# Kernel optimization log

Hardware: AMD Instinct MI355X
Metric: run time of the kernel (lower is better)

## Reference

```python
import jax, jax.numpy as jnp
import numpy as np
from jax import lax

THRESH = 0.6      # pnet score threshold (threshold[0])
IOU_THR = 0.5     # per-scale nms threshold in detect_face
K_PICKS = 128     # fixed max number of NMS picks (jit-static)
STRIDE = 2.0
CELL = 12.0
NEG = -1e30


def _conv(x, w, b):
    y = lax.conv_general_dilated(x, w, (1, 1), 'VALID',
                                 dimension_numbers=('NCHW', 'OIHW', 'NCHW'))
    return y + b[None, :, None, None]


def _prelu(x, a):
    return jnp.where(x > 0, x, a[None, :, None, None] * x)


def _maxpool2(x):
    return lax.reduce_window(x, -jnp.inf, lax.max, (1, 1, 2, 2), (1, 1, 2, 2), 'VALID')


def _nms(boxes, scores):
    # Greedy union-IoU NMS (nms_numpy math), vectorized with a fixed pick budget.
    # boxes [N,4] (shared grid), scores [N] with invalid entries already = NEG.
    x1, y1, x2, y2 = boxes[:, 0], boxes[:, 1], boxes[:, 2], boxes[:, 3]
    area = (x2 - x1 + 1.0) * (y2 - y1 + 1.0)

    def body(live, _):
        j = jnp.argmax(live)
        s = live[j]
        ok = s > NEG * 0.5
        xx1 = jnp.maximum(x1[j], x1); yy1 = jnp.maximum(y1[j], y1)
        xx2 = jnp.minimum(x2[j], x2); yy2 = jnp.minimum(y2[j], y2)
        inter = jnp.maximum(0.0, xx2 - xx1 + 1.0) * jnp.maximum(0.0, yy2 - yy1 + 1.0)
        iou = inter / (area[j] + area - inter)
        live = jnp.where(iou > IOU_THR, NEG, live).at[j].set(NEG)
        return live, (j, ok)

    _, (idx, ok) = lax.scan(body, scores, None, length=K_PICKS)
    return idx, ok


def setup_inputs():
    key = jax.random.key(0)
    ks = jax.random.split(key, 16)
    B, H, W = 16, 384, 512
    f = lambda k, shp, s=0.1: jax.random.normal(k, shp, jnp.float32) * s
    return {
        'im_data': jax.random.uniform(ks[0], (B, 3, H, W), jnp.float32) * 255.0,
        'c1_w': f(ks[1], (10, 3, 3, 3)), 'c1_b': f(ks[2], (10,)),
        'p1': jnp.full((10,), 0.25, jnp.float32),
        'c2_w': f(ks[3], (16, 10, 3, 3)), 'c2_b': f(ks[4], (16,)),
        'p2': jnp.full((16,), 0.25, jnp.float32),
        'c3_w': f(ks[5], (32, 16, 3, 3)), 'c3_b': f(ks[6], (32,)),
        'p3': jnp.full((32,), 0.25, jnp.float32),
        'c41_w': f(ks[7], (2, 32, 1, 1)), 'c41_b': f(ks[8], (2,)),
        'c42_w': f(ks[9], (4, 32, 1, 1)), 'c42_b': f(ks[10], (4,)),
    }


def reference(im_data, c1_w, c1_b, p1, c2_w, c2_b, p2, c3_w, c3_b, p3,
              c41_w, c41_b, c42_w, c42_b):
    # --- PNet conv trunk (detect_face normalization + MTCNN PNet) ---
    x = (im_data - 127.5) * 0.0078125
    h = _prelu(_conv(x, c1_w, c1_b), p1)
    h = _maxpool2(h)                                   # 2x2 s2 (dims even -> ceil==floor)
    h = _prelu(_conv(h, c2_w, c2_b), p2)
    h = _prelu(_conv(h, c3_w, c3_b), p3)
    probs = jax.nn.softmax(_conv(h, c41_w, c41_b), axis=1)[:, 1]   # [B,Hp,Wp]
    reg = _conv(h, c42_w, c42_b)                                   # [B,4,Hp,Wp]

    # --- generateBoundingBox (dense, masked instead of nonzero; scale=1) ---
    B, Hp, Wp = probs.shape
    yy, xx = jnp.meshgrid(jnp.arange(Hp, dtype=jnp.float32),
                          jnp.arange(Wp, dtype=jnp.float32), indexing='ij')
    boxes4 = jnp.stack([jnp.floor(STRIDE * xx + 1.0).ravel(),
                        jnp.floor(STRIDE * yy + 1.0).ravel(),
                        jnp.floor(STRIDE * xx + CELL).ravel(),
                        jnp.floor(STRIDE * yy + CELL).ravel()], axis=1)  # [N,4]
    scores = probs.reshape(B, -1)                                   # [B,N]
    regf = reg.reshape(B, 4, -1).transpose(0, 2, 1)                 # [B,N,4]
    masked = jnp.where(scores >= THRESH, scores, NEG)

    # --- per-image greedy NMS (batched_nms: images independent) ---
    idx, ok = jax.vmap(_nms, in_axes=(None, 0))(boxes4, masked)     # [B,K]
    pb = boxes4[idx]                                                # [B,K,4]
    ps = jnp.take_along_axis(scores, idx, axis=1)                   # [B,K]
    pr = jnp.take_along_axis(regf, idx[..., None], axis=1)          # [B,K,4]

    w = pb[..., 2] - pb[..., 0]
    hh = pb[..., 3] - pb[..., 1]
    q1 = pb[..., 0] + pr[..., 0] * w
    q2 = pb[..., 1] + pr[..., 1] * hh
    q3 = pb[..., 2] + pr[..., 2] * w
    q4 = pb[..., 3] + pr[..., 3] * hh
    rw = q3 - q1
    rh = q4 - q2
    l = jnp.maximum(rw, rh)
    nx1 = q1 + rw * 0.5 - l * 0.5
    ny1 = q2 + rh * 0.5 - l * 0.5
    out = jnp.stack([nx1, ny1, nx1 + l, ny1 + l, ps], axis=-1)      # [B,K,5]
    return out * ok[..., None].astype(out.dtype)
```

## Files before the change

### kernel.cpp

```cpp
#include <hip/hip_runtime.h>
#include <math.h>

#define BATCH 16
#define IH 384
#define IW 512
#define C1 10
#define P1H 191
#define P1W 255
#define C2 16
#define H2 189
#define W2 253
#define C3 32
#define H3 187
#define W3 251
#define N3 (H3*W3)
#define KP 128
#define CAP 7680
#define NEGV (-1e30f)

typedef _Float16 f16x8 __attribute__((ext_vector_type(8)));
typedef _Float16 f16x4 __attribute__((ext_vector_type(4)));
typedef float    f32x16 __attribute__((ext_vector_type(16)));

#define PXT 98
#define NSUB 3

__global__ __launch_bounds__(256, 2) void k_conv1pool(
        const float* __restrict__ im, const float* __restrict__ w,
        const float* __restrict__ bia, const float* __restrict__ slope,
        float* __restrict__ outp) {
    int x = blockIdx.x * 16 + threadIdx.x;
    int y = blockIdx.y * 16 + threadIdx.y;
    int bb = blockIdx.z;
    if (x >= P1W || y >= P1H) return;

    float in[3][4][4];
    #pragma unroll
    for (int ci = 0; ci < 3; ++ci) {
        const float* p = im + (((size_t)bb * 3 + ci) * IH + 2 * y) * IW + 2 * x;
        #pragma unroll
        for (int r = 0; r < 4; ++r) {
            const float2* q = (const float2*)(p + (size_t)r * IW);
            float2 a0 = q[0], a1 = q[1];
            in[ci][r][0] = a0.x; in[ci][r][1] = a0.y;
            in[ci][r][2] = a1.x; in[ci][r][3] = a1.y;
        }
    }
    #pragma unroll
    for (int ci = 0; ci < 3; ++ci)
        #pragma unroll
        for (int r = 0; r < 4; ++r)
            #pragma unroll
            for (int c = 0; c < 4; ++c)
                in[ci][r][c] = (in[ci][r][c] - 127.5f) * 0.0078125f;

    #pragma unroll
    for (int oc = 0; oc < C1; ++oc) {
        const float* wo = w + oc * 27;
        float bv = bia[oc], sv = slope[oc];
        float best = -INFINITY;
        #pragma unroll
        for (int py = 0; py < 2; ++py)
            #pragma unroll
            for (int px = 0; px < 2; ++px) {
                float acc = bv;
                #pragma unroll
                for (int ci = 0; ci < 3; ++ci)
                    #pragma unroll
                    for (int ky = 0; ky < 3; ++ky)
                        #pragma unroll
                        for (int kx = 0; kx < 3; ++kx)
                            acc += in[ci][py + ky][px + kx] * wo[(ci * 3 + ky) * 3 + kx];
                float v = acc > 0.f ? acc : sv * acc;
                best = fmaxf(best, v);
            }
        outp[(((size_t)bb * C1 + oc) * P1H + y) * P1W + x] = best;
    }
}

__global__ __launch_bounds__(256, 2) void k_conv2(
        const float* __restrict__ inp, const float* __restrict__ w,
        const float* __restrict__ bia, const float* __restrict__ slope,
        float* __restrict__ outp) {
    int x0 = (blockIdx.x * 64 + threadIdx.x) * 2;
    int y  = blockIdx.y * 4 + threadIdx.y;
    int bb = blockIdx.z;
    if (x0 >= W2 || y >= H2) return;

    float a0[C2], a1[C2];
    #pragma unroll
    for (int oc = 0; oc < C2; ++oc) { a0[oc] = bia[oc]; a1[oc] = bia[oc]; }

    bool tail = (x0 + 3 > P1W - 1);

    for (int ci = 0; ci < C1; ++ci) {
        const float* p = inp + (((size_t)bb * C1 + ci) * P1H + y) * P1W + x0;
        float v[3][4];
        #pragma unroll
        for (int r = 0; r < 3; ++r) {
            const float* pr = p + (size_t)r * P1W;
            v[r][0] = pr[0]; v[r][1] = pr[1]; v[r][2] = pr[2];
            v[r][3] = tail ? 0.f : pr[3];
        }
        const float* wc = w + ci * 9;
        #pragma unroll
        for (int oc = 0; oc < C2; ++oc) {
            const float* wo = wc + oc * (C1 * 9);
            float s0 = a0[oc], s1 = a1[oc];
            #pragma unroll
            for (int ky = 0; ky < 3; ++ky)
                #pragma unroll
                for (int kx = 0; kx < 3; ++kx) {
                    float wv = wo[ky * 3 + kx];
                    s0 += v[ky][kx]     * wv;
                    s1 += v[ky][kx + 1] * wv;
                }
            a0[oc] = s0; a1[oc] = s1;
        }
    }
    #pragma unroll
    for (int oc = 0; oc < C2; ++oc) {
        float sl = slope[oc];
        float u0 = a0[oc]; a0[oc] = u0 > 0.f ? u0 : sl * u0;
        float u1 = a1[oc]; a1[oc] = u1 > 0.f ? u1 : sl * u1;
    }
    float* o = outp + (((size_t)bb * H2 + y) * W2 + x0) * C2;
    float4* o4 = (float4*)o;
    o4[0] = make_float4(a0[0],  a0[1],  a0[2],  a0[3]);
    o4[1] = make_float4(a0[4],  a0[5],  a0[6],  a0[7]);
    o4[2] = make_float4(a0[8],  a0[9],  a0[10], a0[11]);
    o4[3] = make_float4(a0[12], a0[13], a0[14], a0[15]);
    if (x0 + 1 < W2) {
        float4* p4 = (float4*)(o + C2);
        p4[0] = make_float4(a1[0],  a1[1],  a1[2],  a1[3]);
        p4[1] = make_float4(a1[4],  a1[5],  a1[6],  a1[7]);
        p4[2] = make_float4(a1[8],  a1[9],  a1[10], a1[11]);
        p4[3] = make_float4(a1[12], a1[13], a1[14], a1[15]);
    }
}

__global__ __launch_bounds__(256) void k_prep(const float* __restrict__ w3,
                                              _Float16* __restrict__ wbuf) {
    for (int e = threadIdx.x; e < 4608; e += 256) {
        int oc = e / 144;
        int rem = e - oc * 144;
        int ic = rem / 9;
        int tap = rem - ic * 9;
        float v = w3[e];
        _Float16 h = (_Float16)v;
        _Float16 l = (_Float16)(v - (float)h);
        int d = (tap * 32 + oc) * 16 + ic;
        wbuf[d] = h;
        wbuf[4608 + d] = l;
    }
}

__global__ __launch_bounds__(256, 2) void k_conv3mfma(
        const float* __restrict__ act,
        const _Float16* __restrict__ wbuf,
        const float* __restrict__ b3, const float* __restrict__ s3,
        const float* __restrict__ w41, const float* __restrict__ b41,
        const float* __restrict__ w42, const float* __restrict__ b42,
        float* __restrict__ scores, float4* __restrict__ regf) {
    __shared__ __align__(16) _Float16 Whl[2 * 4608];
    __shared__ __align__(16) _Float16 Ah[6 * PXT * 16];
    __shared__ __align__(16) _Float16 Al[6 * PXT * 16];
    __shared__ __align__(16) float    htab[32 * 8];

    int tid = threadIdx.x;
    int bx = blockIdx.x * (NSUB * 32);
    int by = blockIdx.y * 4;
    int bb = blockIdx.z;

    {
        const float4* src = (const float4*)wbuf;
        float4* dst = (float4*)Whl;
        for (int i = tid; i < 1152; i += 256) dst[i] = src[i];
    }
    {
        int oc = tid >> 3, f = tid & 7;
        float v;
        if      (f == 0) v = b3[oc];
        else if (f == 1) v = s3[oc];
        else if (f == 2) v = w41[oc];
        else if (f == 3) v = w41[32 + oc];
        else             v = w42[(f - 4) * 32 + oc];
        htab[tid] = v;
    }
    {
        const float* actb = act + (size_t)bb * H2 * W2 * C2;
        for (int e = tid; e < 6 * PXT * 4; e += 256) {
            int ic4 = e & 3;
            int t = e >> 2;
            int px = t % PXT;
            int row = t / PXT;
            int yg = by + row, xg = bx + px;
            float4 v = make_float4(0.f, 0.f, 0.f, 0.f);
            if (yg < H2 && xg < W2)
                v = *(const float4*)(actb + ((size_t)yg * W2 + xg) * C2 + ic4 * 4);
            float xs0 = v.x, xs1 = v.y, xs2 = v.z, xs3 = v.w;
            f16x4 hv, lv;
            _Float16 h;
            h = (_Float16)xs0; hv[0] = h; lv[0] = (_Float16)(xs0 - (float)h);
            h = (_Float16)xs1; hv[1] = h; lv[1] = (_Float16)(xs1 - (float)h);
            h = (_Float16)xs2; hv[2] = h; lv[2] = (_Float16)(xs2 - (float)h);
            h = (_Float16)xs3; hv[3] = h; lv[3] = (_Float16)(xs3 - (float)h);
            int d = (row * PXT + px) * 16 + ic4 * 4;
            *(f16x4*)(Ah + d) = hv;
            *(f16x4*)(Al + d) = lv;
        }
    }
    __syncthreads();

    int wv = tid >> 6, lane = tid & 63;
    int col = lane & 31, half = lane >> 5, kg8 = half * 8;
    int y = by + wv;
    if (y >= H3) return;

    f32x16 acc[NSUB];
    #pragma unroll
    for (int s = 0; s < NSUB; ++s)
        #pragma unroll
        for (int i = 0; i < 16; ++i) acc[s][i] = 0.f;

    #pragma unroll
    for (int ky = 0; ky < 3; ++ky) {
        const _Float16* arh = Ah + (wv + ky) * (PXT * 16);
        const _Float16* arl = Al + (wv + ky) * (PXT * 16);
        #pragma unroll
        for (int kx = 0; kx < 3; ++kx) {
            int tap = ky * 3 + kx;
            f16x8 wh = *(const f16x8*)(Whl + (tap * 32 + col) * 16 + kg8);
            f16x8 wl = *(const f16x8*)(Whl + 4608 + (tap * 32 + col) * 16 + kg8);
            #pragma unroll
            for (int s = 0; s < NSUB; ++s) {
                int p = s * 32 + col + kx;
                f16x8 bh = *(const f16x8*)(arh + p * 16 + kg8);
                f16x8 bl = *(const f16x8*)(arl + p * 16 + kg8);
                acc[s] = __builtin_amdgcn_mfma_f32_32x32x16_f16(wh, bh, acc[s], 0, 0, 0);
                acc[s] = __builtin_amdgcn_mfma_f32_32x32x16_f16(wl, bh, acc[s], 0, 0, 0);
                acc[s] = __builtin_amdgcn_mfma_f32_32x32x16_f16(wh, bl, acc[s], 0, 0, 0);
            }
        }
    }

    float L0[NSUB], L1[NSUB], R0[NSUB], R1[NSUB], R2[NSUB], R3[NSUB];
    #pragma unroll
    for (int s = 0; s < NSUB; ++s) { L0[s]=0.f; L1[s]=0.f; R0[s]=0.f; R1[s]=0.f; R2[s]=0.f; R3[s]=0.f; }

    #pragma unroll
    for (int r = 0; r < 16; ++r) {
        int oc = (r & 3) + 8 * (r >> 2) + 4 * half;
        float4 t0 = *(const float4*)&htab[oc * 8];
        float4 t1 = *(const float4*)&htab[oc * 8 + 4];
        #pragma unroll
        for (int s = 0; s < NSUB; ++s) {
            float v = acc[s][r] + t0.x;
            v = v > 0.f ? v : v * t0.y;
            L0[s] += v * t0.z; L1[s] += v * t0.w;
            R0[s] += v * t1.x; R1[s] += v * t1.y;
            R2[s] += v * t1.z; R3[s] += v * t1.w;
        }
    }

    float hb0 = b41[0], hb1 = b41[1];
    float rb0 = b42[0], rb1 = b42[1], rb2 = b42[2], rb3 = b42[3];

    #pragma unroll
    for (int s = 0; s < NSUB; ++s) {
        float l0 = L0[s] + __shfl_xor(L0[s], 32) + hb0;
        float l1 = L1[s] + __shfl_xor(L1[s], 32) + hb1;
        float r0 = R0[s] + __shfl_xor(R0[s], 32) + rb0;
        float r1 = R1[s] + __shfl_xor(R1[s], 32) + rb1;
        float r2 = R2[s] + __shfl_xor(R2[s], 32) + rb2;
        float r3 = R3[s] + __shfl_xor(R3[s], 32) + rb3;
        float m = fmaxf(l0, l1);
        float e0 = expf(l0 - m), e1 = expf(l1 - m);
        float p = e1 / (e0 + e1);
        int px = bx + s * 32 + col;
        if (half == 0 && px < W3) {
            size_t n = (size_t)bb * N3 + (size_t)y * W3 + px;
            scores[n] = (p >= 0.6f) ? p : NEGV;
            regf[n] = make_float4(r0, r1, r2, r3);
        }
    }
}

__global__ __launch_bounds__(1024) void k_nms(
        const float* __restrict__ scores, const float4* __restrict__ regf,
        float* __restrict__ outp) {
    __shared__ float s_score[CAP];
    __shared__ int   s_idx[CAP];
    __shared__ float r_s[16];
    __shared__ int   r_i[16];
    __shared__ float s_picks[KP];
    __shared__ int   s_picki[KP];
    __shared__ int   s_misc[4];

    int tid = threadIdx.x;
    int bb = blockIdx.x;
    const float* sc = scores + (size_t)bb * N3;

    if (tid < 4) s_misc[tid] = 0;
    __syncthreads();

    int cnt = 0;
    for (int i = tid; i < N3; i += 1024) if (sc[i] > 0.f) cnt++;
    atomicAdd(&s_misc[0], cnt);
    __syncthreads();
    int M = s_misc[0];

    int cutbin = 0;
    if (M > CAP) {
        for (int i = tid; i < 2048; i += 1024) s_idx[i] = 0;
        __syncthreads();
        for (int i = tid; i < N3; i += 1024) {
            float s = sc[i];
            if (s > 0.f) {
                int b = (int)((s - 0.6f) * 5120.f);
                b = b < 0 ? 0 : (b > 2047 ? 2047 : b);
                atomicAdd(&s_idx[b], 1);
            }
        }
        __syncthreads();
        if (tid == 0) {
            int accum = 0, b = 2047;
            for (; b >= 0; --b) {
                int c = s_idx[b];
                if (accum + c > CAP) break;
                accum += c;
            }
            s_misc[2] = b + 1;
        }
        __syncthreads();
        cutbin = s_misc[2];
        __syncthreads();
    }

    for (int i = tid; i < N3; i += 1024) {
        float s = sc[i];
        if (s > 0.f) {
            bool keep = true;
            if (M > CAP) {
                int b = (int)((s - 0.6f) * 5120.f);
                b = b < 0 ? 0 : (b > 2047 ? 2047 : b);
                keep = (b >= cutbin);
            }
            if (keep) {
                int pos = atomicAdd(&s_misc[1], 1);
                if (pos < CAP) { s_score[pos] = s; s_idx[pos] = i; }
            }
        }
    }
    __syncthreads();
    int M2 = s_misc[1]; if (M2 > CAP) M2 = CAP;

    int np = 0;
    for (int pick = 0; pick < KP; ++pick) {
        float bs = -INFINITY; int bi = 0x7fffffff;
        for (int i = tid; i < M2; i += 1024) {
            float s = s_score[i]; int id = s_idx[i];
            if (s > bs || (s == bs && id < bi)) { bs = s; bi = id; }
        }
        #pragma unroll
        for (int off = 32; off; off >>= 1) {
            float os = __shfl_down(bs, off);
            int   oi = __shfl_down(bi, off);
            if (os > bs || (os == bs && oi < bi)) { bs = os; bi = oi; }
        }
        int lane = tid & 63, wv = tid >> 6;
        if (lane == 0) { r_s[wv] = bs; r_i[wv] = bi; }
        __syncthreads();
        if (tid == 0) {
            float ps = r_s[0]; int pi = r_i[0];
            for (int k = 1; k < 16; ++k) {
                float os = r_s[k]; int oi = r_i[k];
                if (os > ps || (os == ps && oi < pi)) { ps = os; pi = oi; }
            }
            s_picks[pick] = ps; s_picki[pick] = pi;
            r_s[0] = ps; r_i[0] = pi;
        }
        __syncthreads();
        float ps = r_s[0]; int pi = r_i[0];
        if (ps < 0.f) break;
        np = pick + 1;

        int pcx = pi % W3, pcy = pi / W3;
        float px1 = (float)(2 * pcx + 1), py1 = (float)(2 * pcy + 1);
        float px2 = (float)(2 * pcx + 12), py2 = (float)(2 * pcy + 12);
        for (int i = tid; i < M2; i += 1024) {
            float s = s_score[i];
            if (s > NEGV * 0.5f) {
                int id = s_idx[i];
                int cx = id % W3, cy = id / W3;
                float x1 = (float)(2 * cx + 1), y1 = (float)(2 * cy + 1);
                float x2 = (float)(2 * cx + 12), y2 = (float)(2 * cy + 12);
                float xx1 = fmaxf(px1, x1), yy1 = fmaxf(py1, y1);
                float xx2 = fminf(px2, x2), yy2 = fminf(py2, y2);
                float inter = fmaxf(0.f, xx2 - xx1 + 1.f) * fmaxf(0.f, yy2 - yy1 + 1.f);
                float iou = inter / (288.f - inter);
                if (iou > 0.5f) s_score[i] = NEGV;
            }
        }
        __syncthreads();
    }

    if (tid < KP) {
        float* o = outp + ((size_t)bb * KP + tid) * 5;
        if (tid < np) {
            int pi = s_picki[tid]; float ps = s_picks[tid];
            int cx = pi % W3, cy = pi / W3;
            float x1 = (float)(2 * cx + 1), y1 = (float)(2 * cy + 1);
            float x2 = (float)(2 * cx + 12), y2 = (float)(2 * cy + 12);
            float4 r = regf[(size_t)bb * N3 + pi];
            float wd = x2 - x1, hh = y2 - y1;
            float q1 = x1 + r.x * wd, q2 = y1 + r.y * hh;
            float q3 = x2 + r.z * wd, q4 = y2 + r.w * hh;
            float rw = q3 - q1, rh = q4 - q2;
            float L = fmaxf(rw, rh);
            float nx1 = q1 + rw * 0.5f - L * 0.5f;
            float ny1 = q2 + rh * 0.5f - L * 0.5f;
            o[0] = nx1; o[1] = ny1; o[2] = nx1 + L; o[3] = ny1 + L; o[4] = ps;
        } else {
            o[0] = 0.f; o[1] = 0.f; o[2] = 0.f; o[3] = 0.f; o[4] = 0.f;
        }
    }
}

extern "C" void kernel_launch(void* const* d_in, const int* in_sizes, int n_in,
                              void* d_out, int out_size, void* d_ws, size_t ws_size,
                              hipStream_t stream) {
    const float* im   = (const float*)d_in[0];
    const float* c1w  = (const float*)d_in[1];
    const float* c1b  = (const float*)d_in[2];
    const float* p1   = (const float*)d_in[3];
    const float* c2w  = (const float*)d_in[4];
    const float* c2b  = (const float*)d_in[5];
    const float* p2   = (const float*)d_in[6];
    const float* c3w  = (const float*)d_in[7];
    const float* c3b  = (const float*)d_in[8];
    const float* p3   = (const float*)d_in[9];
    const float* c41w = (const float*)d_in[10];
    const float* c41b = (const float*)d_in[11];
    const float* c42w = (const float*)d_in[12];
    const float* c42b = (const float*)d_in[13];

    float* ws = (float*)d_ws;
    const size_t POOL1_FLOATS = (size_t)BATCH * C1 * P1H * P1W;
    float*  pool1  = ws;
    float*  conv2b = ws + POOL1_FLOATS;
    float*  scoresb = ws;
    float4* regfb   = (float4*)(ws + (size_t)BATCH * N3);
    _Float16* wbuf = (_Float16*)d_out;

    k_prep<<<dim3(1), dim3(256), 0, stream>>>(c3w, wbuf);
    k_conv1pool<<<dim3(16, 12, BATCH), dim3(16, 16), 0, stream>>>(im, c1w, c1b, p1, pool1);
    k_conv2   <<<dim3(2, 48, BATCH), dim3(64, 4), 0, stream>>>(pool1, c2w, c2b, p2, conv2b);
    k_conv3mfma<<<dim3(3, 47, BATCH), dim3(256), 0, stream>>>(conv2b, wbuf, c3b, p3,
                                                              c41w, c41b, c42w, c42b,
                                                              scoresb, regfb);
    k_nms<<<dim3(BATCH), dim3(1024), 0, stream>>>(scoresb, regfb, (float*)d_out);
}
```

Before: 244.8 us.

## Fuse weight prep into conv1, stage conv2 stores via LDS, stream conv3 weights from global

The separate weight-prep launch is folded into the first block of conv1, removing one kernel launch. conv2 now stages its outputs through a swizzled shared buffer so global stores are coalesced float4 writes. conv3 stops copying the split-f16 weights into LDS and reads them straight from global memory in a new k-split layout. Activation LDS is reorganised to match, which frees shared memory and raises occupancy to 4 blocks, at the cost of global weight loads inside the MFMA loop and a non-unrolled ky loop.

```diff
diff --git a/kernel.cpp b/kernel.cpp
--- a/kernel.cpp
+++ b/kernel.cpp
@@ -28,7 +28,24 @@
 __global__ __launch_bounds__(256, 2) void k_conv1pool(
         const float* __restrict__ im, const float* __restrict__ w,
         const float* __restrict__ bia, const float* __restrict__ slope,
-        float* __restrict__ outp) {
+        float* __restrict__ outp,
+        const float* __restrict__ w3, _Float16* __restrict__ wbuf) {
+    if (blockIdx.x == 0 && blockIdx.y == 0 && blockIdx.z == 0) {
+        int tid = threadIdx.y * 16 + threadIdx.x;
+        for (int e = tid; e < 4608; e += 256) {
+            int oc = e / 144;
+            int rem = e - oc * 144;
+            int ic = rem / 9;
+            int tap = rem - ic * 9;
+            float v = w3[e];
+            _Float16 h = (_Float16)v;
+            _Float16 l = (_Float16)(v - (float)h);
+            int d = ((tap * 2 + (ic >> 3)) * 32 + oc) * 8 + (ic & 7);
+            wbuf[d] = h;
+            wbuf[4608 + d] = l;
+        }
+    }
+
     int x = blockIdx.x * 16 + threadIdx.x;
     int y = blockIdx.y * 16 + threadIdx.y;
     int bb = blockIdx.z;
@@ -82,89 +99,86 @@
         const float* __restrict__ inp, const float* __restrict__ w,
         const float* __restrict__ bia, const float* __restrict__ slope,
         float* __restrict__ outp) {
-    int x0 = (blockIdx.x * 64 + threadIdx.x) * 2;
-    int y  = blockIdx.y * 4 + threadIdx.y;
+    __shared__ float4 sbuf[2048];
+    int tx = threadIdx.x, ty = threadIdx.y;
+    int tid = ty * 64 + tx;
+    int x0 = blockIdx.x * 128 + tx * 2;
+    int y  = blockIdx.y * 4 + ty;
     int bb = blockIdx.z;
-    if (x0 >= W2 || y >= H2) return;
+    bool alive = (x0 < W2) && (y < H2);
 
     float a0[C2], a1[C2];
     #pragma unroll
     for (int oc = 0; oc < C2; ++oc) { a0[oc] = bia[oc]; a1[oc] = bia[oc]; }
 
-    bool tail = (x0 + 3 > P1W - 1);
-
-    for (int ci = 0; ci < C1; ++ci) {
-        const float* p = inp + (((size_t)bb * C1 + ci) * P1H + y) * P1W + x0;
-        float v[3][4];
-        #pragma unroll
-        for (int r = 0; r < 3; ++r) {
-            const float* pr = p + (size_t)r * P1W;
-            v[r][0] = pr[0]; v[r][1] = pr[1]; v[r][2] = pr[2];
-            v[r][3] = tail ? 0.f : pr[3];
-        }
-        const float* wc = w + ci * 9;
+    if (alive) {
+        bool tail = (x0 + 3 > P1W - 1);
+        for (int ci = 0; ci < C1; ++ci) {
+            const float* p = inp + (((size_t)bb * C1 + ci) * P1H + y) * P1W + x0;
+            float v[3][4];
+            #pragma unroll
+            for (int r = 0; r < 3; ++r) {
+                const float* pr = p + (size_t)r * P1W;
+                v[r][0] = pr[0]; v[r][1] = pr[1]; v[r][2] = pr[2];
+                v[r][3] = tail ? 0.f : pr[3];
+            }
+            const float* wc = w + ci * 9;
+            #pragma unroll
+            for (int oc = 0; oc < C2; ++oc) {
+                const float* wo = wc + oc * (C1 * 9);
+                float s0 = a0[oc], s1 = a1[oc];
+                #pragma unroll
+                for (int ky = 0; ky < 3; ++ky)
+                    #pragma unroll
+                    for (int kx = 0; kx < 3; ++kx) {
+                        float wv = wo[ky * 3 + kx];
+                        s0 += v[ky][kx]     * wv;
+                        s1 += v[ky][kx + 1] * wv;
+                    }
+                a0[oc] = s0; a1[oc] = s1;
+            }
+        }
         #pragma unroll
         for (int oc = 0; oc < C2; ++oc) {
-            const float* wo = wc + oc * (C1 * 9);
-            float s0 = a0[oc], s1 = a1[oc];
-            #pragma unroll
-            for (int ky = 0; ky < 3; ++ky)
-                #pragma unroll
-                for (int kx = 0; kx < 3; ++kx) {
-                    float wv = wo[ky * 3 + kx];
-                    s0 += v[ky][kx]     * wv;
-                    s1 += v[ky][kx + 1] * wv;
-                }
-            a0[oc] = s0; a1[oc] = s1;
-        }
-    }
-    #pragma unroll
-    for (int oc = 0; oc < C2; ++oc) {
-        float sl = slope[oc];
-        float u0 = a0[oc]; a0[oc] = u0 > 0.f ? u0 : sl * u0;
-        float u1 = a1[oc]; a1[oc] = u1 > 0.f ? u1 : sl * u1;
-    }
-    float* o = outp + (((size_t)bb * H2 + y) * W2 + x0) * C2;
-    float4* o4 = (float4*)o;
-    o4[0] = make_float4(a0[0],  a0[1],  a0[2],  a0[3]);
-    o4[1] = make_float4(a0[4],  a0[5],  a0[6],  a0[7]);
-    o4[2] = make_float4(a0[8],  a0[9],  a0[10], a0[11]);
-    o4[3] = make_float4(a0[12], a0[13], a0[14], a0[15]);
-    if (x0 + 1 < W2) {
-        float4* p4 = (float4*)(o + C2);
-        p4[0] = make_float4(a1[0],  a1[1],  a1[2],  a1[3]);
-        p4[1] = make_float4(a1[4],  a1[5],  a1[6],  a1[7]);
-        p4[2] = make_float4(a1[8],  a1[9],  a1[10], a1[11]);
-        p4[3] = make_float4(a1[12], a1[13], a1[14], a1[15]);
+            float sl = slope[oc];
+            float u0 = a0[oc]; a0[oc] = u0 > 0.f ? u0 : sl * u0;
+            float u1 = a1[oc]; a1[oc] = u1 > 0.f ? u1 : sl * u1;
+        }
+    }
+
+    #pragma unroll
+    for (int c4 = 0; c4 < 4; ++c4) {
+        int g0 = tid * 8 + c4;
+        int p0 = g0 ^ ((g0 >> 3) & 7);
+        sbuf[p0] = make_float4(a0[c4 * 4], a0[c4 * 4 + 1], a0[c4 * 4 + 2], a0[c4 * 4 + 3]);
+        int g1 = tid * 8 + 4 + c4;
+        int p1 = g1 ^ ((g1 >> 3) & 7);
+        sbuf[p1] = make_float4(a1[c4 * 4], a1[c4 * 4 + 1], a1[c4 * 4 + 2], a1[c4 * 4 + 3]);
+    }
+    __syncthreads();
+
+    const size_t obase = (size_t)bb * H2 * W2 * C2;
+    #pragma unroll
+    for (int it = 0; it < 8; ++it) {
+        int g = it * 256 + tid;
+        int c4 = g & 3, px = (g >> 2) & 127, ry = g >> 9;
+        int xg = blockIdx.x * 128 + px, yg = blockIdx.y * 4 + ry;
+        if (xg < W2 && yg < H2) {
+            int phys = g ^ ((g >> 3) & 7);
+            *(float4*)(outp + obase + ((size_t)yg * W2 + xg) * C2 + c4 * 4) = sbuf[phys];
+        }
     }
 }
 
-__global__ __launch_bounds__(256) void k_prep(const float* __restrict__ w3,
-                                              _Float16* __restrict__ wbuf) {
-    for (int e = threadIdx.x; e < 4608; e += 256) {
-        int oc = e / 144;
-        int rem = e - oc * 144;
-        int ic = rem / 9;
-        int tap = rem - ic * 9;
-        float v = w3[e];
-        _Float16 h = (_Float16)v;
-        _Float16 l = (_Float16)(v - (float)h);
-        int d = (tap * 32 + oc) * 16 + ic;
-        wbuf[d] = h;
-        wbuf[4608 + d] = l;
-    }
-}
-
-__global__ __launch_bounds__(256, 2) void k_conv3mfma(
+__global__ __launch_bounds__(256, 4) void k_conv3mfma(
         const float* __restrict__ act,
         const _Float16* __restrict__ wbuf,
         const float* __restrict__ b3, const float* __restrict__ s3,
         const float* __restrict__ w41, const float* __restrict__ b41,
         const float* __restrict__ w42, const float* __restrict__ b42,
         float* __restrict__ scores, float4* __restrict__ regf) {
-    __shared__ __align__(16) _Float16 Whl[2 * 4608];
-    __shared__ __align__(16) _Float16 Ah[6 * PXT * 16];
-    __shared__ __align__(16) _Float16 Al[6 * PXT * 16];
+    __shared__ __align__(16) _Float16 Ah[6 * 2 * PXT * 8];
+    __shared__ __align__(16) _Float16 Al[6 * 2 * PXT * 8];
     __shared__ __align__(16) float    htab[32 * 8];
 
     int tid = threadIdx.x;
@@ -172,11 +186,6 @@
     int by = blockIdx.y * 4;
     int bb = blockIdx.z;
 
-    {
-        const float4* src = (const float4*)wbuf;
-        float4* dst = (float4*)Whl;
-        for (int i = tid; i < 1152; i += 256) dst[i] = src[i];
-    }
     {
         int oc = tid >> 3, f = tid & 7;
         float v;
@@ -205,15 +214,16 @@
             h = (_Float16)xs1; hv[1] = h; lv[1] = (_Float16)(xs1 - (float)h);
             h = (_Float16)xs2; hv[2] = h; lv[2] = (_Float16)(xs2 - (float)h);
             h = (_Float16)xs3; hv[3] = h; lv[3] = (_Float16)(xs3 - (float)h);
-            int d = (row * PXT + px) * 16 + ic4 * 4;
-            *(f16x4*)(Ah + d) = hv;
-            *(f16x4*)(Al + d) = lv;
+            int kg = ic4 >> 1, h4 = ic4 & 1;
+            int gr = (row * 2 + kg) * PXT + px;
+            *(f16x4*)(Ah + gr * 8 + h4 * 4) = hv;
+            *(f16x4*)(Al + gr * 8 + h4 * 4) = lv;
         }
     }
     __syncthreads();
 
     int wv = tid >> 6, lane = tid & 63;
-    int col = lane & 31, half = lane >> 5, kg8 = half * 8;
+    int col = lane & 31, half = lane >> 5;
     int y = by + wv;
     if (y >= H3) return;
 
@@ -223,20 +233,22 @@
         #pragma unroll
         for (int i = 0; i < 16; ++i) acc[s][i] = 0.f;
 
-    #pragma unroll
+    const _Float16* wg = wbuf + (half * 32 + col) * 8;
+
+    #pragma unroll 1
     for (int ky = 0; ky < 3; ++ky) {
-        const _Float16* arh = Ah + (wv + ky) * (PXT * 16);
-        const _Float16* arl = Al + (wv + ky) * (PXT * 16);
+        const _Float16* arh = Ah + ((wv + ky) * 2 + half) * (PXT * 8);
+        const _Float16* arl = Al + ((wv + ky) * 2 + half) * (PXT * 8);
         #pragma unroll
         for (int kx = 0; kx < 3; ++kx) {
             int tap = ky * 3 + kx;
-            f16x8 wh = *(const f16x8*)(Whl + (tap * 32 + col) * 16 + kg8);
-            f16x8 wl = *(const f16x8*)(Whl + 4608 + (tap * 32 + col) * 16 + kg8);
+            f16x8 wh = *(const f16x8*)(wg + tap * 512);
+            f16x8 wl = *(const f16x8*)(wg + 4608 + tap * 512);
             #pragma unroll
             for (int s = 0; s < NSUB; ++s) {
                 int p = s * 32 + col + kx;
-                f16x8 bh = *(const f16x8*)(arh + p * 16 + kg8);
-                f16x8 bl = *(const f16x8*)(arl + p * 16 + kg8);
+                f16x8 bh = *(const f16x8*)(arh + p * 8);
+                f16x8 bl = *(const f16x8*)(arl + p * 8);
                 acc[s] = __builtin_amdgcn_mfma_f32_32x32x16_f16(wh, bh, acc[s], 0, 0, 0);
                 acc[s] = __builtin_amdgcn_mfma_f32_32x32x16_f16(wl, bh, acc[s], 0, 0, 0);
                 acc[s] = __builtin_amdgcn_mfma_f32_32x32x16_f16(wh, bl, acc[s], 0, 0, 0);
@@ -453,8 +465,8 @@
     float4* regfb   = (float4*)(ws + (size_t)BATCH * N3);
     _Float16* wbuf = (_Float16*)d_out;
 
-    k_prep<<<dim3(1), dim3(256), 0, stream>>>(c3w, wbuf);
-    k_conv1pool<<<dim3(16, 12, BATCH), dim3(16, 16), 0, stream>>>(im, c1w, c1b, p1, pool1);
+    k_conv1pool<<<dim3(16, 12, BATCH), dim3(16, 16), 0, stream>>>(im, c1w, c1b, p1, pool1,
+                                                                  c3w, wbuf);
     k_conv2   <<<dim3(2, 48, BATCH), dim3(64, 4), 0, stream>>>(pool1, c2w, c2b, p2, conv2b);
     k_conv3mfma<<<dim3(3, 47, BATCH), dim3(256), 0, stream>>>(conv2b, wbuf, c3b, p3,
                                                               c41w, c41b, c42w, c42b,
```

Measured after the change: 287.6 us. +17.5%, slower.
